# Performance work log

Hardware: AMD Instinct MI355X
Metric: run time of the kernel (lower is better)

The kernel has to match this reference:

```python
import jax, jax.numpy as jnp
import numpy as np

W = 8          # block window width
R = 4          # block stride (upsampling ratio)
STRICT_CAUSAL = False
EPS = 1e-8


def _triangular_kernel(w_len: int) -> jnp.ndarray:
    # matches torch: up=linspace(0,1,W//2+1); w=cat(up[:-1], flip(up)) -> length W+1 for even W
    up = jnp.linspace(0.0, 1.0, w_len // 2 + 1)
    w = jnp.concatenate([up[:-1], up[::-1]])
    if w.shape[0] < w_len:  # static pad (only for odd W edge cases)
        w = jnp.concatenate([w, jnp.full((w_len - w.shape[0],), w[-1])])
    return w


def _overlap_matrix(S: int, N: int, kernel: jnp.ndarray, dtype) -> jnp.ndarray:
    # A[t, i] = kernel[t - i*R] if 0 <= t - i*R <= W-1 (band), then row-normalized.
    t = jnp.arange(S)[:, None]              # [S,1]
    s = jnp.arange(N)[None, :] * R          # [1,N] block starts
    off = t - s                             # [S,N]
    valid = (off >= 0) & (off <= W - 1)
    if STRICT_CAUSAL:
        valid = valid & (t >= s + W - 1)    # only t >= block end
    vals = kernel[jnp.clip(off, 0, W - 1)].astype(dtype)
    A = jnp.where(valid, vals, jnp.zeros((), dtype))
    A = A / (A.sum(axis=1, keepdims=True) + EPS)
    return A


def setup_inputs() -> dict:
    key = jax.random.key(0)
    B, N, H = 4, 2048, 1024
    Z = jax.random.normal(key, (B, N, H), dtype=jnp.float32)
    return {"Z": Z, "S_out": 8192}


def reference(Z, S_out):
    B, N, H = Z.shape
    kernel = _triangular_kernel(W)
    A = _overlap_matrix(S_out, N, kernel, Z.dtype)   # [S,N] banded, row-normalized
    return jnp.einsum('sn,bnh->bsh', A, Z)           # [B,S,H]
```

## Files before the change

### kernel.cpp

```cpp
#include <hip/hip_runtime.h>


#define B_DIM 4
#define N_DIM 2048
#define H4    256
#define S_DIM 8192

__global__ __launch_bounds__(256)
void Upscaler_33294586479031_kernel(const float4* __restrict__ Z,
                                    float4* __restrict__ out) {
    const int bid = blockIdx.x;
    const int q   = bid & (N_DIM - 1);
    const int b   = bid >> 11;
    const int h   = threadIdx.x;

    const float4* zb = Z + (size_t)b * N_DIM * H4;
    float4* ob = out + (size_t)b * S_DIM * H4 + (size_t)(4 * q) * H4 + h;

    const float4 zq = zb[(size_t)q * H4 + h];

    if (q == 0) {
        float4 zero; zero.x = zero.y = zero.z = zero.w = 0.0f;
        ob[0 * H4] = zero;
        ob[1 * H4] = zq;
        ob[2 * H4] = zq;
        ob[3 * H4] = zq;
    } else {
        const float4 zp = zb[(size_t)(q - 1) * H4 + h];
        #pragma unroll
        for (int m = 0; m < 4; ++m) {
            const float w1 = 0.25f * (float)m;
            const float w0 = 1.0f - w1;
            float4 r;
            r.x = w0 * zp.x + w1 * zq.x;
            r.y = w0 * zp.y + w1 * zq.y;
            r.z = w0 * zp.z + w1 * zq.z;
            r.w = w0 * zp.w + w1 * zq.w;
            ob[m * H4] = r;
        }
    }
}

extern "C" void kernel_launch(void* const* d_in, const int* in_sizes, int n_in,
                              void* d_out, int out_size, void* d_ws, size_t ws_size,
                              hipStream_t stream) {
    const float4* Z  = (const float4*)d_in[0];
    float4* out      = (float4*)d_out;

    const int grid = B_DIM * N_DIM;
    Upscaler_33294586479031_kernel<<<grid, 256, 0, stream>>>(Z, out);
}
```

Measured before the change: 154.9 us.

## Process two input rows per block with XCD swizzle and nontemporal stores

Each block now handles two consecutive input rows, loading three rows instead of two per row and writing eight output rows, so the grid is halved and redundant input reads drop. Block IDs are remapped so that each of the eight XCDs gets a contiguous chunk of work, which is meant to improve L2 locality for the shared neighbouring rows. Output writes use nontemporal stores to avoid polluting cache with the streaming output. The kernel is already bandwidth-bound and writes dominate, so the gain may be small.

```diff
diff --git a/kernel.cpp b/kernel.cpp
--- a/kernel.cpp
+++ b/kernel.cpp
@@ -1,52 +1,66 @@
 #include <hip/hip_runtime.h>
 
+
+typedef float f4 __attribute__((ext_vector_type(4)));
 
 #define B_DIM 4
 #define N_DIM 2048
 #define H4    256
 #define S_DIM 8192
+#define NBLK  (B_DIM * (N_DIM / 2))
+#define NXCD  8
+#define CHUNK (NBLK / NXCD)
 
 __global__ __launch_bounds__(256)
-void Upscaler_33294586479031_kernel(const float4* __restrict__ Z,
-                                    float4* __restrict__ out) {
+void Upscaler_33294586479031_kernel(const f4* __restrict__ Z,
+                                    f4* __restrict__ out) {
     const int bid = blockIdx.x;
-    const int q   = bid & (N_DIM - 1);
-    const int b   = bid >> 11;
-    const int h   = threadIdx.x;
+    const int swz = (bid & (NXCD - 1)) * CHUNK + (bid >> 3);
 
-    const float4* zb = Z + (size_t)b * N_DIM * H4;
-    float4* ob = out + (size_t)b * S_DIM * H4 + (size_t)(4 * q) * H4 + h;
+    const int q2 = swz & (N_DIM / 2 - 1);
+    const int b  = swz >> 10;
+    const int h  = threadIdx.x;
+    const int q0 = q2 * 2;
 
-    const float4 zq = zb[(size_t)q * H4 + h];
+    const f4* zbase = Z + (size_t)b * (N_DIM * H4) + h;
 
-    if (q == 0) {
-        float4 zero; zero.x = zero.y = zero.z = zero.w = 0.0f;
-        ob[0 * H4] = zero;
-        ob[1 * H4] = zq;
-        ob[2 * H4] = zq;
-        ob[3 * H4] = zq;
+    const int qm = (q0 > 0) ? (q0 - 1) : 0;
+    const f4 zm = zbase[(size_t)qm * H4];
+    const f4 z0 = zbase[(size_t)q0 * H4];
+    const f4 z1 = zbase[(size_t)(q0 + 1) * H4];
+
+    f4* ob = out + (size_t)b * (S_DIM * H4) + (size_t)(4 * q0) * H4 + h;
+
+    if (q0 == 0) {
+        const f4 zero = (f4)(0.0f);
+        __builtin_nontemporal_store(zero, &ob[0 * H4]);
+        __builtin_nontemporal_store(z0,   &ob[1 * H4]);
+        __builtin_nontemporal_store(z0,   &ob[2 * H4]);
+        __builtin_nontemporal_store(z0,   &ob[3 * H4]);
     } else {
-        const float4 zp = zb[(size_t)(q - 1) * H4 + h];
         #pragma unroll
         for (int m = 0; m < 4; ++m) {
             const float w1 = 0.25f * (float)m;
             const float w0 = 1.0f - w1;
-            float4 r;
-            r.x = w0 * zp.x + w1 * zq.x;
-            r.y = w0 * zp.y + w1 * zq.y;
-            r.z = w0 * zp.z + w1 * zq.z;
-            r.w = w0 * zp.w + w1 * zq.w;
-            ob[m * H4] = r;
+            const f4 r = w0 * zm + w1 * z0;
+            __builtin_nontemporal_store(r, &ob[m * H4]);
         }
+    }
+
+    #pragma unroll
+    for (int m = 0; m < 4; ++m) {
+        const float w1 = 0.25f * (float)m;
+        const float w0 = 1.0f - w1;
+        const f4 r = w0 * z0 + w1 * z1;
+        __builtin_nontemporal_store(r, &ob[(4 + m) * H4]);
     }
 }
 
 extern "C" void kernel_launch(void* const* d_in, const int* in_sizes, int n_in,
                               void* d_out, int out_size, void* d_ws, size_t ws_size,
                               hipStream_t stream) {
-    const float4* Z  = (const float4*)d_in[0];
-    float4* out      = (float4*)d_out;
+    const f4* Z = (const f4*)d_in[0];
+    f4* out     = (f4*)d_out;
 
-    const int grid = B_DIM * N_DIM;
-    Upscaler_33294586479031_kernel<<<grid, 256, 0, stream>>>(Z, out);
+    Upscaler_33294586479031_kernel<<<NBLK, 256, 0, stream>>>(Z, out);
 }
```

Result: slower. 165.7 us (+7.0%).
